# Optimization experiments

Measured on AMD Instinct MI355X. Metric: run time of the kernel, lower is better.

Reference implementation:

```python
import jax, jax.numpy as jnp
import numpy as np
from jax import lax

B, H, W, CL, CC, CD, NH, NP = 8, 48, 48, 384, 384, 384, 12, 4
N = H * W
HD = CL // NH
SCALE = HD ** -0.5


def _pool_mat(n, out=7):
    # torch AdaptiveAvgPool2d bin edges: [floor(i*n/out), ceil((i+1)*n/out))
    M = np.zeros((out, n), np.float32)
    for i in range(out):
        s = (i * n) // out
        e = -(-((i + 1) * n) // out)
        M[i, s:e] = 1.0 / (e - s)
    return jnp.asarray(M)


def _resize_mat(out_n, in_n):
    # bilinear, align_corners=False (torch F.interpolate)
    M = np.zeros((out_n, in_n), np.float32)
    scale = in_n / out_n
    for o in range(out_n):
        src = (o + 0.5) * scale - 0.5
        src = min(max(src, 0.0), in_n - 1.0)
        i0 = int(np.floor(src))
        i1 = min(i0 + 1, in_n - 1)
        f = src - i0
        M[o, i0] += 1.0 - f
        M[o, i1] += f
    return jnp.asarray(M)


def _ln_c(x, g, b):
    # LayerNorm over channel dim of NCHW, eps=1e-6
    mu = jnp.mean(x, axis=1, keepdims=True)
    var = jnp.mean((x - mu) ** 2, axis=1, keepdims=True)
    xn = (x - mu) * lax.rsqrt(var + 1e-6)
    return xn * g[None, :, None, None] + b[None, :, None, None]


def _c1(x, w):
    # 1x1 conv, w: (out,in)
    return jnp.einsum('oc,bchw->bohw', w, x)


def _bilerp(feat, grid):
    # feat (G,C,Hs,Ws), grid (G,M,2) xy in [-1,1]; align_corners=False, zero padding
    G, C, Hs, Ws = feat.shape
    x = (grid[..., 0] + 1.0) * 0.5 * Ws - 0.5
    y = (grid[..., 1] + 1.0) * 0.5 * Hs - 0.5
    x0 = jnp.floor(x)
    y0 = jnp.floor(y)
    fx = x - x0
    fy = y - y0
    featf = feat.transpose(0, 2, 3, 1).reshape(G, Hs * Ws, C)
    x0i = x0.astype(jnp.int32)
    y0i = y0.astype(jnp.int32)

    def corner(ix, iy):
        valid = ((ix >= 0) & (ix < Ws) & (iy >= 0) & (iy < Hs)).astype(feat.dtype)
        flat = jnp.clip(iy, 0, Hs - 1) * Ws + jnp.clip(ix, 0, Ws - 1)
        g = jax.vmap(lambda f, i: f[i])(featf, flat)  # (G,M,C)
        return g * valid[..., None]

    v00 = corner(x0i, y0i)
    v01 = corner(x0i + 1, y0i)
    v10 = corner(x0i, y0i + 1)
    v11 = corner(x0i + 1, y0i + 1)
    w00 = ((1 - fx) * (1 - fy))[..., None]
    w01 = (fx * (1 - fy))[..., None]
    w10 = ((1 - fx) * fy)[..., None]
    w11 = (fx * fy)[..., None]
    return v00 * w00 + v01 * w01 + v10 * w10 + v11 * w11  # (G,M,C)


def _forward(local_feat, context_prior, deformable_x, W_q, W_k, W_v, W_pre, ln1_g, ln1_b,
             W_post, dw_w, dw_b, ln2_g, ln2_b, W_lo, b_lo, W_off, b_off,
             attention_biases, W_p, bn_g, bn_b, bn_mean, bn_var):
    q = _c1(local_feat, W_q)  # (B,CL,H,W)

    # context_offset_guide: 1x1 -> GELU -> adaptive pool 7x7 -> LN(C) -> 1x1 to 32 -> resize
    cg = jax.nn.gelu(_c1(context_prior, W_pre), approximate=False)
    Mh, Mw = _pool_mat(H), _pool_mat(W)
    pooled = jnp.einsum('oh,pw,bchw->bcop', Mh, Mw, cg)
    guide = _c1(_ln_c(pooled, ln1_g, ln1_b), W_post)  # (B,32,7,7)
    Uh, Uw = _resize_mat(H, 7), _resize_mat(W, 7)
    guide = jnp.einsum('Oh,Pw,bchw->bcOP', Uh, Uw, guide)  # (B,32,H,W)

    # local_offset_base: dwconv3x3 -> LN(C) -> GELU -> 1x1 to 32
    dw = lax.conv_general_dilated(local_feat, dw_w, (1, 1), [(1, 1), (1, 1)],
                                  dimension_numbers=('NCHW', 'OIHW', 'NCHW'),
                                  feature_group_count=CL) + dw_b[None, :, None, None]
    lo = jax.nn.gelu(_ln_c(dw, ln2_g, ln2_b), approximate=False)
    lo = _c1(lo, W_lo) + b_lo[None, :, None, None]  # (B,32,H,W)

    fused = jnp.concatenate([guide, lo], axis=1)  # (B,64,H,W)
    off = _c1(fused, W_off) + b_off[None, :, None, None]  # (B,NH*NP*2,H,W)
    off = off.transpose(0, 2, 3, 1).reshape(B, H, W, NH, NP, 2)
    offn = off / jnp.asarray([W, H], dtype=off.dtype)

    ry = (jnp.arange(H, dtype=off.dtype) + 0.5) / H
    rx = (jnp.arange(W, dtype=off.dtype) + 0.5) / W
    ref = jnp.stack([jnp.broadcast_to(rx[None, :], (H, W)),
                     jnp.broadcast_to(ry[:, None], (H, W))], axis=-1)  # (H,W,2) xy
    grid = (ref[None, :, :, None, None, :] + offn) * 2.0 - 1.0  # (B,H,W,NH,NP,2)

    gridh = grid.reshape(B, N, NH, NP, 2).transpose(0, 2, 1, 3, 4)  # (B,NH,N,NP,2)
    grid_r = gridh.reshape(B * NH, N * NP, 2)

    k = _c1(context_prior, W_k).reshape(B * NH, HD, H, W)
    v = _c1(deformable_x, W_v).reshape(B * NH, HD, H, W)
    k_s = _bilerp(k, grid_r).reshape(B, NH, N, NP, HD)
    v_s = _bilerp(v, grid_r).reshape(B, NH, N, NP, HD)

    qh = q.reshape(B, NH, HD, N).transpose(0, 1, 3, 2)  # (B,NH,N,HD)
    scores = jnp.einsum('bhnd,bhnpd->bhnp', qh, k_s) * SCALE

    # relative position bias: idx(p1,p2) = |dy|*W + |dx| (first-seen enumeration)
    px = jnp.clip(jnp.round((gridh[..., 0] + 1.0) * 0.5 * W - 0.5), 0, W - 1).astype(jnp.int32)
    py = jnp.clip(jnp.round((gridh[..., 1] + 1.0) * 0.5 * H - 0.5), 0, H - 1).astype(jnp.int32)
    n = jnp.arange(N, dtype=jnp.int32)
    qy = (n // W)[None, None, :, None]
    qx = (n % W)[None, None, :, None]
    bidx = jnp.abs(qy - py) * W + jnp.abs(qx - px)  # (B,NH,N,NP)
    bias = attention_biases[jnp.arange(NH)[None, :, None, None], bidx]

    attn = jax.nn.softmax(scores + bias, axis=-1)
    out = jnp.einsum('bhnp,bhnpd->bhnd', attn, v_s)  # (B,NH,N,HD)
    out = out.transpose(0, 1, 3, 2).reshape(B, CL, H, W)

    y = _c1(out, W_p)
    y = bn_g[None, :, None, None] * (y - bn_mean[None, :, None, None]) * \
        lax.rsqrt(bn_var[None, :, None, None] + 1e-5) + bn_b[None, :, None, None]
    return y


def setup_inputs():
    ks = jax.random.split(jax.random.key(0), 16)
    f32 = jnp.float32
    d = {
        'local_feat': jax.random.normal(ks[0], (B, CL, H, W), f32),
        'context_prior': jax.random.normal(ks[1], (B, CC, H, W), f32),
        'deformable_x': jax.random.normal(ks[2], (B, CD, H, W), f32),
        'W_q': jax.random.normal(ks[3], (CL, CL), f32) * 0.02,
        'W_k': jax.random.normal(ks[4], (CL, CC), f32) * 0.02,
        'W_v': jax.random.normal(ks[5], (CD, CD), f32) * 0.02,
        'W_pre': jax.random.normal(ks[6], (CC, CC), f32) * 0.02,
        'ln1_g': jnp.ones((CC,), f32),
        'ln1_b': jnp.zeros((CC,), f32),
        'W_post': jax.random.normal(ks[7], (32, CC), f32) * 0.02,
        'dw_w': jax.random.normal(ks[8], (CL, 1, 3, 3), f32) * 0.1,
        'dw_b': jnp.zeros((CL,), f32),
        'ln2_g': jnp.ones((CL,), f32),
        'ln2_b': jnp.zeros((CL,), f32),
        'W_lo': jax.random.normal(ks[9], (32, CL), f32) * 0.02,
        'b_lo': jnp.zeros((32,), f32),
        'W_off': jax.random.normal(ks[10], (NH * NP * 2, 64), f32) * 0.01,
        'b_off': jax.random.normal(ks[11], (NH * NP * 2,), f32) * 0.5,
        'attention_biases': jax.random.normal(ks[12], (NH, H * W), f32) * 0.02,
        'W_p': jax.random.normal(ks[13], (CL, CL), f32) * 0.02,
        'bn_g': jnp.ones((CL,), f32),
        'bn_b': jnp.zeros((CL,), f32),
        'bn_mean': jax.random.normal(ks[14], (CL,), f32) * 0.01,
        'bn_var': jax.random.uniform(ks[15], (CL,), f32, 0.5, 1.5),
    }
    return d


def reference(local_feat, context_prior, deformable_x, W_q, W_k, W_v, W_pre, ln1_g, ln1_b,
              W_post, dw_w, dw_b, ln2_g, ln2_b, W_lo, b_lo, W_off, b_off,
              attention_biases, W_p, bn_g, bn_b, bn_mean, bn_var):
    return _forward(local_feat, context_prior, deformable_x, W_q, W_k, W_v, W_pre, ln1_g,
                    ln1_b, W_post, dw_w, dw_b, ln2_g, ln2_b, W_lo, b_lo, W_off, b_off,
                    attention_biases, W_p, bn_g, bn_b, bn_mean, bn_var)
```

## Files before the change

### kernel.cpp

```cpp
#include <hip/hip_runtime.h>
#include <hip/hip_bf16.h>
#include <math.h>

#define B_ 8
#define H_ 48
#define W_ 48
#define N_ 2304
#define C_ 384
#define NH_ 12
#define NP_ 4
#define HD_ 32
#define SCALE_ 0.17677669529663687f

typedef unsigned short ushort;
typedef short bf16x8 __attribute__((ext_vector_type(8)));
typedef float f32x4 __attribute__((ext_vector_type(4)));

__device__ __forceinline__ float b2f(ushort u) {
    union { float f; unsigned i; } x; x.i = ((unsigned)u) << 16; return x.f;
}
__device__ __forceinline__ ushort f2b(float f) {
    __hip_bfloat16 h = __float2bfloat16(f);
    return *(ushort*)&h;
}
__device__ __forceinline__ float ldin(const void* p, size_t i, int isbf) {
    return isbf ? b2f(((const ushort*)p)[i]) : ((const float*)p)[i];
}
__device__ __forceinline__ float geluf(float x) {
    return 0.5f * x * (1.0f + erff(x * 0.70710678118654752440f));
}
__device__ __forceinline__ int iabs(int x) { return x < 0 ? -x : x; }
__device__ __forceinline__ int get_isbf(const void* lnq) {
    return (*(const unsigned*)lnq == 0x3F803F80u) ? 1 : 0;
}

__device__ __forceinline__ void gl_lds16(const ushort* g, ushort* l) {
    __builtin_amdgcn_global_load_lds(
        (const __attribute__((address_space(1))) unsigned int*)g,
        (__attribute__((address_space(3))) unsigned int*)l, 16, 0, 0);
}

#define PREP_MAX 24
struct PrepTab {
    const void* src[PREP_MAX];
    void*       dst[PREP_MAX];
    int         n[PREP_MAX];
    int         tobf[PREP_MAX];
};
struct TPtrs { const void* src[3]; ushort* dst[3]; };
struct SetupRaw {
    const void* WoffRaw;
    const void* WloRaw;
    const void* bloRaw;
    const void* boffRaw;
    const void* dwRaw;
    const void* lnq;
    ushort* Bext;
    float*  biasp;
    float*  dwwT;
};

__global__ __launch_bounds__(256) void setup_kernel(TPtrs tp, PrepTab tab, int ne, SetupRaw rw)
{
    const int isbf = get_isbf(rw.lnq);
    const int tid = threadIdx.x;
    const int bid = blockIdx.x;
    const int DWT0 = ne * 8;
    const int WC0  = DWT0 + 2;
    const int T30  = WC0 + 96;

    if (bid < DWT0) {
        const int e = bid >> 3, sub = bid & 7;
        const int n = tab.n[e];
        const void* src = tab.src[e];
        if (tab.tobf[e]) {
            ushort* dst = (ushort*)tab.dst[e];
            if (isbf) {
                const ushort* s = (const ushort*)src;
                for (int i = sub * 256 + tid; i < n; i += 8 * 256) dst[i] = s[i];
            } else {
                const float* s = (const float*)src;
                for (int i = sub * 256 + tid; i < n; i += 8 * 256) dst[i] = f2b(s[i]);
            }
        } else {
            float* dst = (float*)tab.dst[e];
            if (isbf) {
                const ushort* s = (const ushort*)src;
                for (int i = sub * 256 + tid; i < n; i += 8 * 256) dst[i] = b2f(s[i]);
            } else {
                const float* s = (const float*)src;
                for (int i = sub * 256 + tid; i < n; i += 8 * 256) dst[i] = s[i];
            }
        }
    } else if (bid < WC0) {
        const int c = (bid - DWT0) * 256 + tid;
        if (c < C_) {
#pragma unroll
            for (int u = 0; u < 9; u++)
                rw.dwwT[u * C_ + c] = ldin(rw.dwRaw, (size_t)c * 9 + u, isbf);
        }
    } else if (bid < T30) {
        const int co = bid - WC0;
        for (int c = tid; c < C_; c += 256) {
            float acc = 0.f;
#pragma unroll 8
            for (int j = 0; j < 32; j++)
                acc += ldin(rw.WoffRaw, (size_t)co * 64 + 32 + j, isbf)
                     * ldin(rw.WloRaw, (size_t)j * 384 + c, isbf);
            ushort hi = f2b(acc);
            float r = acc - b2f(hi);
            ushort lo = f2b(r);
            rw.Bext[co * 1152 + c] = hi;
            rw.Bext[co * 1152 + 384 + c] = lo;
            rw.Bext[co * 1152 + 768 + c] = hi;
        }
        if (tid == 0) {
            float bp = ldin(rw.boffRaw, co, isbf);
            for (int j = 0; j < 32; j++)
                bp += ldin(rw.WoffRaw, (size_t)co * 64 + 32 + j, isbf)
                    * ldin(rw.bloRaw, j, isbf);
            rw.biasp[co] = bp;
        }
    } else {
        const int t3 = bid - T30;
        const int x = t3 % 36;
        const int rem = t3 / 36;
        const int y = rem % 12;
        const int z = rem / 12;
        const int which = z >> 3;
        const int b = z & 7;
        const int n0 = x * 64, c0 = y * 32;
        const void* in = tp.src[which];
        ushort* out = tp.dst[which];
        const int t = tid;

        __shared__ unsigned tile[64][33];

        if (isbf) {
            {
                const int c = t >> 3, s = t & 7;
                uint4 v = *(const uint4*)((const ushort*)in + ((size_t)b * C_ + c0 + c) * N_ + n0 + s * 8);
                const int nb = s * 8;
                tile[nb + 0][c] = v.x & 0xffff; tile[nb + 1][c] = v.x >> 16;
                tile[nb + 2][c] = v.y & 0xffff; tile[nb + 3][c] = v.y >> 16;
                tile[nb + 4][c] = v.z & 0xffff; tile[nb + 5][c] = v.z >> 16;
                tile[nb + 6][c] = v.w & 0xffff; tile[nb + 7][c] = v.w >> 16;
            }
            __syncthreads();
            {
                const int n = t >> 2, s = t & 3;
                const int cb = s * 8;
                unsigned p0 = tile[n][cb + 0] | (tile[n][cb + 1] << 16);
                unsigned p1 = tile[n][cb + 2] | (tile[n][cb + 3] << 16);
                unsigned p2 = tile[n][cb + 4] | (tile[n][cb + 5] << 16);
                unsigned p3 = tile[n][cb + 6] | (tile[n][cb + 7] << 16);
                uint4 o; o.x = p0; o.y = p1; o.z = p2; o.w = p3;
                *(uint4*)(out + ((size_t)b * N_ + n0 + n) * C_ + c0 + cb) = o;
            }
        } else {
            float* tf = (float*)&tile[0][0];
            const int tx = t & 31, ty = t >> 5;
            for (int sub = 0; sub < 2; sub++) {
                int ns = n0 + sub * 32;
                __syncthreads();
#pragma unroll
                for (int u = 0; u < 4; u++) {
                    int c = ty + u * 8;
                    tf[c * 33 + tx] = ((const float*)in)[((size_t)b * C_ + c0 + c) * N_ + ns + tx];
                }
                __syncthreads();
#pragma unroll
                for (int u = 0; u < 4; u++) {
                    int n = ty + u * 8;
                    out[((size_t)b * N_ + ns + n) * C_ + c0 + tx] = f2b(tf[tx * 33 + n]);
                }
            }
        }
    }
}

struct QKV4Ptrs { const ushort* A[4]; const ushort* Bw[4]; void* Y[4]; };
__global__ __launch_bounds__(256, 3) void mega_gemm_kernel(
    QKV4Ptrs qp,
    const ushort* __restrict__ AHI, const ushort* __restrict__ ALO,
    const ushort* __restrict__ Bext, float* __restrict__ OFFP)
{
    __shared__ ushort As[3][128 * 32];
    __shared__ ushort Bs[3][128 * 32];
    const int tid = threadIdx.x;
    const int lane = tid & 63, wave = tid >> 6;
    const int wr = wave >> 1, wc = wave & 1;
    const int quad = lane >> 4, l15 = lane & 15;
    const int bid = blockIdx.x;

    if (bid < 144) {
        const int m0 = bid * 128;

        f32x4 acc[4][3];
#pragma unroll
        for (int i = 0; i < 4; i++)
#pragma unroll
            for (int j = 0; j < 3; j++) acc[i][j] = (f32x4){0.f, 0.f, 0.f, 0.f};

        auto stage = [&](int p, int t) {
            const int seg = t / 12;
            const ushort* Ag = (seg < 2) ? AHI : ALO;
            const int acol = t * 32 - seg * 384;
            const int bcol = t * 32;
#pragma unroll
            for (int u = 0; u < 2; u++) {
                int idx = tid + 256 * u;
                int r = idx >> 2, s = idx & 3;
                int rb = r < 96 ? r : 95;
                gl_lds16(Ag + (size_t)(m0 + r) * 384 + acol + 8 * s, &As[p][idx * 8]);
                gl_lds16(Bext + (size_t)rb * 1152 + bcol + 8 * s, &Bs[p][idx * 8]);
            }
        };

        stage(0, 0);
        stage(1, 1);
        const int nt = 36;
        for (int t = 0; t < nt; ++t) {
            if (t + 1 < nt) asm volatile("s_waitcnt vmcnt(4)" ::: "memory");
            else            asm volatile("s_waitcnt vmcnt(0)" ::: "memory");
            __builtin_amdgcn_s_barrier();
            __builtin_amdgcn_sched_barrier(0);
            if (t + 2 < nt) stage((t + 2) % 3, t + 2);
            const int p = t % 3;
            bf16x8 af[4], bfr[3];
#pragma unroll
            for (int i = 0; i < 4; i++)
                af[i]  = *(const bf16x8*)&As[p][(wr * 64 + i * 16 + l15) * 32 + quad * 8];
#pragma unroll
            for (int j = 0; j < 3; j++)
                bfr[j] = *(const bf16x8*)&Bs[p][(wc * 48 + j * 16 + l15) * 32 + quad * 8];
#pragma unroll
            for (int i = 0; i < 4; i++)
#pragma unroll
                for (int j = 0; j < 3; j++)
                    acc[i][j] = __builtin_amdgcn_mfma_f32_16x16x32_bf16(af[i], bfr[j], acc[i][j], 0, 0, 0);
        }

#pragma unroll
        for (int i = 0; i < 4; i++) {
#pragma unroll
            for (int r = 0; r < 4; r++) {
                int m = m0 + wr * 64 + i * 16 + quad * 4 + r;
#pragma unroll
                for (int j = 0; j < 3; j++) {
                    int co = wc * 48 + j * 16 + l15;
                    OFFP[(size_t)m * 96 + co] = acc[i][j][r];
                }
            }
        }
    } else {
        const int q = bid - 144;
        const int zc = q / 54, r2 = q % 54;
        const int which = zc >> 3, b = zc & 7;
        const int m0 = (r2 / 3) * 128;
        const int n0 = (r2 % 3) * 128;
        const ushort* Ag = qp.A[which];
        const ushort* Bg = qp.Bw[which];

        f32x4 acc[4][4];
#pragma unroll
        for (int i = 0; i < 4; i++)
#pragma unroll
            for (int j = 0; j < 4; j++) acc[i][j] = (f32x4){0.f, 0.f, 0.f, 0.f};

        const size_t abase = (size_t)b * (size_t)N_ * C_;

        auto stage = [&](int p, int kc) {
#pragma unroll
            for (int u = 0; u < 2; u++) {
                int idx = tid + 256 * u;
                int r = idx >> 2, s = idx & 3;
                gl_lds16(Ag + abase + (size_t)(m0 + r) * C_ + kc + 8 * s, &As[p][idx * 8]);
                gl_lds16(Bg + (size_t)(n0 + r) * C_ + kc + 8 * s, &Bs[p][idx * 8]);
            }
        };

        stage(0, 0);
        stage(1, 32);
        const int nt = C_ / 32;
        for (int t = 0; t < nt; ++t) {
            if (t + 1 < nt) asm volatile("s_waitcnt vmcnt(4)" ::: "memory");
            else            asm volatile("s_waitcnt vmcnt(0)" ::: "memory");
            __builtin_amdgcn_s_barrier();
            __builtin_amdgcn_sched_barrier(0);
            if (t + 2 < nt) stage((t + 2) % 3, (t + 2) * 32);
            const int p = t % 3;
            bf16x8 af[4], bfr[4];
#pragma unroll
            for (int i = 0; i < 4; i++)
                af[i]  = *(const bf16x8*)&As[p][(wr * 64 + i * 16 + l15) * 32 + quad * 8];
#pragma unroll
            for (int j = 0; j < 4; j++)
                bfr[j] = *(const bf16x8*)&Bs[p][(wc * 64 + j * 16 + l15) * 32 + quad * 8];
#pragma unroll
            for (int i = 0; i < 4; i++)
#pragma unroll
                for (int j = 0; j < 4; j++)
                    acc[i][j] = __builtin_amdgcn_mfma_f32_16x16x32_bf16(af[i], bfr[j], acc[i][j], 0, 0, 0);
        }

        ushort* Yg = (ushort*)qp.Y[which];
        if (which < 3) {
#pragma unroll
            for (int i = 0; i < 4; i++) {
#pragma unroll
                for (int r = 0; r < 4; r++) {
                    int m = m0 + wr * 64 + i * 16 + quad * 4 + r;
#pragma unroll
                    for (int j = 0; j < 4; j++) {
                        int nn = n0 + wc * 64 + j * 16 + l15;
                        Yg[abase + (size_t)m * C_ + nn] = f2b(acc[i][j][r]);
                    }
                }
            }
        } else {
#pragma unroll
            for (int i = 0; i < 4; i++) {
#pragma unroll
                for (int r = 0; r < 4; r++) {
                    int m = m0 + wr * 64 + i * 16 + quad * 4 + r;
#pragma unroll
                    for (int j = 0; j < 4; j++) {
                        int nn = n0 + wc * 64 + j * 16 + l15;
                        Yg[abase + (size_t)m * C_ + nn] = f2b(geluf(acc[i][j][r]));
                    }
                }
            }
        }
    }
}

__global__ __launch_bounds__(256, 4) void gemm_final_kernel(
    const ushort* __restrict__ WpB, const ushort* __restrict__ AOut,
    void* __restrict__ Yg,
    const float* __restrict__ bng, const float* __restrict__ bnb,
    const float* __restrict__ bnm, const float* __restrict__ bnv,
    const void* __restrict__ lnq)
{
    const int isbf = get_isbf(lnq);
    const int l = (blockIdx.x & 7) * 108 + (blockIdx.x >> 3);
    const int b = l / 108, r2 = l % 108;
    const int n0 = (r2 / 3) * 64;
    const int m0 = (r2 % 3) * 128;

    __shared__ ushort As[3][128 * 32];
    __shared__ ushort Bs[3][64 * 32];
    const int tid = threadIdx.x;
    const int lane = tid & 63, wave = tid >> 6;
    const int quad = lane >> 4, l15 = lane & 15;
    const int sx = (quad ^ (l15 & 3)) * 8;

    f32x4 acc[2][4];
#pragma unroll
    for (int i = 0; i < 2; i++)
#pragma unroll
        for (int j = 0; j < 4; j++) acc[i][j] = (f32x4){0.f, 0.f, 0.f, 0.f};

    const size_t bbase = (size_t)b * (size_t)N_ * C_;

    auto stage = [&](int p, int kc) {
#pragma unroll
        for (int u = 0; u < 2; u++) {
            int idx = tid + 256 * u;
            int r = idx >> 2, sl = idx & 3;
            int sg = sl ^ (r & 3);
            gl_lds16(WpB + (size_t)(m0 + r) * C_ + kc + 8 * sg, &As[p][idx * 8]);
        }
        {
            int r = tid >> 2, sl = tid & 3;
            int sg = sl ^ (r & 3);
            gl_lds16(AOut + bbase + (size_t)(n0 + r) * C_ + kc + 8 * sg, &Bs[p][tid * 8]);
        }
    };

    stage(0, 0);
    stage(1, 32);

    const int nt = C_ / 32;
    for (int t = 0; t < nt; ++t) {
        if (t + 1 < nt) asm volatile("s_waitcnt vmcnt(3)" ::: "memory");
        else            asm volatile("s_waitcnt vmcnt(0)" ::: "memory");
        __builtin_amdgcn_s_barrier();
        __builtin_amdgcn_sched_barrier(0);
        if (t + 2 < nt) stage((t + 2) % 3, (t + 2) * 32);
        const int p = t % 3;
        bf16x8 af[2], bfr[4];
#pragma unroll
        for (int i = 0; i < 2; i++)
            af[i]  = *(const bf16x8*)&As[p][(wave * 32 + i * 16 + l15) * 32 + sx];
#pragma unroll
        for (int j = 0; j < 4; j++)
            bfr[j] = *(const bf16x8*)&Bs[p][(j * 16 + l15) * 32 + sx];
#pragma unroll
        for (int i = 0; i < 2; i++)
#pragma unroll
            for (int j = 0; j < 4; j++)
                acc[i][j] = __builtin_amdgcn_mfma_f32_16x16x32_bf16(af[i], bfr[j], acc[i][j], 0, 0, 0);
    }

    const size_t ybase = (size_t)b * (size_t)C_ * N_;
#pragma unroll
    for (int i = 0; i < 2; i++) {
#pragma unroll
        for (int r = 0; r < 4; r++) {
            int m = m0 + wave * 32 + i * 16 + quad * 4 + r;
            float sc = bng[m] * rsqrtf(bnv[m] + 1e-5f);
            float sh = bnb[m] - sc * bnm[m];
#pragma unroll
            for (int j = 0; j < 4; j++) {
                int nn = n0 + j * 16 + l15;
                float v = sc * acc[i][j][r] + sh;
                size_t yi = ybase + (size_t)m * N_ + nn;
                if (isbf) ((ushort*)Yg)[yi] = f2b(v);
                else ((float*)Yg)[yi] = v;
            }
        }
    }
}

__global__ __launch_bounds__(384) void pool_ln_guide_kernel(
    const ushort* __restrict__ CG, const float* __restrict__ g, const float* __restrict__ bt,
    const ushort* __restrict__ WpostB, const ushort* __restrict__ WoffB,
    float* __restrict__ OG7)
{
    const int cell = blockIdx.x % 49, b = blockIdx.x / 49;
    const int i = cell / 7, j = cell % 7, c = threadIdx.x;
    const int sh = (i * H_) / 7, eh = ((i + 1) * H_ + 6) / 7;
    const int sw = (j * W_) / 7, ew = ((j + 1) * W_ + 6) / 7;
    float s = 0.f;
    for (int h = sh; h < eh; h++)
        for (int w = sw; w < ew; w++)
            s += b2f(CG[((size_t)b * N_ + h * W_ + w) * C_ + c]);
    s *= 1.0f / (float)((eh - sh) * (ew - sw));

    float rs = s, rq = s * s;
#pragma unroll
    for (int m = 1; m <= 32; m <<= 1) {
        rs += __shfl_xor(rs, m);
        rq += __shfl_xor(rq, m);
    }
    __shared__ float ss[6], sq[6], buf[C_];
    __shared__ float psum[12][33];
    __shared__ float g7s[32];
    int wid = threadIdx.x >> 6;
    if ((threadIdx.x & 63) == 0) { ss[wid] = rs; sq[wid] = rq; }
    __syncthreads();
    if (threadIdx.x == 0) {
        float ts = 0.f, tq = 0.f;
        for (int k = 0; k < 6; k++) { ts += ss[k]; tq += sq[k]; }
        ss[0] = ts; sq[0] = tq;
    }
    __syncthreads();
    float mu = ss[0] / (float)C_;
    float var = sq[0] / (float)C_ - mu * mu;
    float inv = rsqrtf(var + 1e-6f);
    buf[c] = (s - mu) * inv * g[c] + bt[c];
    __syncthreads();

    const int oc = threadIdx.x & 31, seg = threadIdx.x >> 5;
    const uint4* wp = (const uint4*)(WpostB + oc * C_ + seg * 32);
    float part = 0.f;
#pragma unroll
    for (int u = 0; u < 4; u++) {
        uint4 v = wp[u];
        const float* bb = &buf[seg * 32 + u * 8];
        part += b2f((ushort)(v.x & 0xffff)) * bb[0] + b2f((ushort)(v.x >> 16)) * bb[1];
        part += b2f((ushort)(v.y & 0xffff)) * bb[2] + b2f((ushort)(v.y >> 16)) * bb[3];
        part += b2f((ushort)(v.z & 0xffff)) * bb[4] + b2f((ushort)(v.z >> 16)) * bb[5];
        part += b2f((ushort)(v.w & 0xffff)) * bb[6] + b2f((ushort)(v.w >> 16)) * bb[7];
    }
    psum[seg][oc] = part;
    __syncthreads();
    if (threadIdx.x < 32) {
        float acc = 0.f;
#pragma unroll
        for (int k = 0; k < 12; k++) acc += psum[k][threadIdx.x];
        g7s[threadIdx.x] = acc;
    }
    __syncthreads();
    if (threadIdx.x < 96) {
        const int co = threadIdx.x;
        float acc = 0.f;
#pragma unroll 8
        for (int k = 0; k < 32; k++)
            acc += b2f(WoffB[co * 64 + k]) * g7s[k];
        OG7[(size_t)blockIdx.x * 96 + co] = acc;
    }
}

__global__ __launch_bounds__(512) void dw_ln_gelu_kernel(
    const ushort* __restrict__ LF, const float* __restrict__ WdT, const float* __restrict__ BdF,
    const float* __restrict__ g, const float* __restrict__ bt,
    ushort* __restrict__ AHI, ushort* __restrict__ ALO)
{
    const int wave = threadIdx.x >> 6, lane = threadIdx.x & 63;
    const int m = blockIdx.x * 8 + wave;
    const int b = m / N_, n = m % N_;
    const int h = n / W_, w = n % W_;
    const bool act = lane < 48;
    const int c0 = lane * 8;

    float acc[8];
#pragma unroll
    for (int j = 0; j < 8; j++) acc[j] = 0.f;
    if (act) {
        f32x4 b0 = *(const f32x4*)(BdF + c0);
        f32x4 b1 = *(const f32x4*)(BdF + c0 + 4);
#pragma unroll
        for (int j = 0; j < 4; j++) { acc[j] = b0[j]; acc[4 + j] = b1[j]; }
    }

#pragma unroll
    for (int u = 0; u < 9; u++) {
        const int ky = u / 3, kx = u % 3;
        const int y = h + ky - 1, x = w + kx - 1;
        if (act && y >= 0 && y < H_ && x >= 0 && x < W_) {
            uint4 v = *(const uint4*)(LF + ((size_t)b * N_ + y * W_ + x) * C_ + c0);
            f32x4 wa = *(const f32x4*)(WdT + u * C_ + c0);
            f32x4 wb = *(const f32x4*)(WdT + u * C_ + c0 + 4);
            acc[0] += wa[0] * b2f((ushort)(v.x & 0xffff));
            acc[1] += wa[1] * b2f((ushort)(v.x >> 16));
            acc[2] += wa[2] * b2f((ushort)(v.y & 0xffff));
            acc[3] += wa[3] * b2f((ushort)(v.y >> 16));
            acc[4] += wb[0] * b2f((ushort)(v.z & 0xffff));
            acc[5] += wb[1] * b2f((ushort)(v.z >> 16));
            acc[6] += wb[2] * b2f((ushort)(v.w & 0xffff));
            acc[7] += wb[3] * b2f((ushort)(v.w >> 16));
        }
    }

    float rs = 0.f, rq = 0.f;
#pragma unroll
    for (int j = 0; j < 8; j++) { rs += acc[j]; rq += acc[j] * acc[j]; }
#pragma unroll
    for (int s = 1; s <= 32; s <<= 1) {
        rs += __shfl_xor(rs, s);
        rq += __shfl_xor(rq, s);
    }
    float mu = rs / (float)C_;
    float var = rq / (float)C_ - mu * mu;
    float inv = rsqrtf(var + 1e-6f);

    if (act) {
        f32x4 g0 = *(const f32x4*)(g + c0);
        f32x4 g1 = *(const f32x4*)(g + c0 + 4);
        f32x4 t0 = *(const f32x4*)(bt + c0);
        f32x4 t1 = *(const f32x4*)(bt + c0 + 4);
        float v[8];
#pragma unroll
        for (int j = 0; j < 4; j++) {
            v[j]     = geluf((acc[j]     - mu) * inv * g0[j] + t0[j]);
            v[4 + j] = geluf((acc[4 + j] - mu) * inv * g1[j] + t1[j]);
        }
        uint4 hi, lo;
        ushort hs[8], ls[8];
#pragma unroll
        for (int j = 0; j < 8; j++) {
            hs[j] = f2b(v[j]);
            ls[j] = f2b(v[j] - b2f(hs[j]));
        }
        hi.x = (unsigned)hs[0] | ((unsigned)hs[1] << 16);
        hi.y = (unsigned)hs[2] | ((unsigned)hs[3] << 16);
        hi.z = (unsigned)hs[4] | ((unsigned)hs[5] << 16);
        hi.w = (unsigned)hs[6] | ((unsigned)hs[7] << 16);
        lo.x = (unsigned)ls[0] | ((unsigned)ls[1] << 16);
        lo.y = (unsigned)ls[2] | ((unsigned)ls[3] << 16);
        lo.z = (unsigned)ls[4] | ((unsigned)ls[5] << 16);
        lo.w = (unsigned)ls[6] | ((unsigned)ls[7] << 16);
        size_t idx = (size_t)m * C_ + c0;
        *(uint4*)(AHI + idx) = hi;
        *(uint4*)(ALO + idx) = lo;
    }
}

__global__ __launch_bounds__(384) void attn_kernel(
    const ushort* __restrict__ Q, const ushort* __restrict__ K, const ushort* __restrict__ V,
    const float* __restrict__ OFFP, const float* __restrict__ biasp,
    const float* __restrict__ OG7,
    const float* __restrict__ ABf, ushort* __restrict__ OUT)
{
    const int pairi = blockIdx.x;
    const int b = pairi / (N_ / 2);
    const int n0 = (pairi % (N_ / 2)) * 2;
    const int tid = threadIdx.x;

    __shared__ int   cidxS[96][4];
    __shared__ float cwS[96][4];
    __shared__ float biasS[96];

    if (tid < 96) {
        const int pos = tid / 48, idx = tid % 48;
        const int n = n0 + pos;
        const int h = n / W_, w = n % W_;
        const int nh = idx >> 2, p = idx & 3;
        const int co = nh * 8 + 2 * p;

        const float fs = 7.0f / 48.0f;
        float sy = fminf(fmaxf(((float)h + 0.5f) * fs - 0.5f, 0.f), 6.f);
        float sx = fminf(fmaxf(((float)w + 0.5f) * fs - 0.5f, 0.f), 6.f);
        int gy0 = (int)floorf(sy), gx0 = (int)floorf(sx);
        int gy1 = min(gy0 + 1, 6), gx1 = min(gx0 + 1, 6);
        float gfy = sy - (float)gy0, gfx = sx - (float)gx0;
        float bw00 = (1.f - gfy) * (1.f - gfx), bw01 = (1.f - gfy) * gfx;
        float bw10 = gfy * (1.f - gfx), bw11 = gfy * gfx;
        const float* ogb = OG7 + (size_t)b * 49 * 96;
        int c00 = (gy0 * 7 + gx0) * 96, c01 = (gy0 * 7 + gx1) * 96;
        int c10 = (gy1 * 7 + gx0) * 96, c11 = (gy1 * 7 + gx1) * 96;
        const size_t mrow = ((size_t)b * N_ + n) * 96;

        float ox = OFFP[mrow + co] + biasp[co]
                 + bw00 * ogb[c00 + co] + bw01 * ogb[c01 + co]
                 + bw10 * ogb[c10 + co] + bw11 * ogb[c11 + co];
        float oy = OFFP[mrow + co + 1] + biasp[co + 1]
                 + bw00 * ogb[c00 + co + 1] + bw01 * ogb[c01 + co + 1]
                 + bw10 * ogb[c10 + co + 1] + bw11 * ogb[c11 + co + 1];

        float x = (float)w + ox;
        float y = (float)h + oy;

        int px = (int)fminf(fmaxf(rintf(x), 0.f), (float)(W_ - 1));
        int py = (int)fminf(fmaxf(rintf(y), 0.f), (float)(H_ - 1));
        biasS[tid] = ABf[(size_t)nh * N_ + iabs(h - py) * W_ + iabs(w - px)];

        float x0f = floorf(x), y0f = floorf(y);
        float fx = x - x0f, fy = y - y0f;
        int x0 = (int)x0f, y0 = (int)y0f;
#pragma unroll
        for (int cc = 0; cc < 4; cc++) {
            int dx = cc & 1, dy = cc >> 1;
            int ix = x0 + dx, iy = y0 + dy;
            bool valid = (ix >= 0) && (ix < W_) && (iy >= 0) && (iy < H_);
            int ixc = min(max(ix, 0), W_ - 1), iyc = min(max(iy, 0), H_ - 1);
            cidxS[tid][cc] = iyc * W_ + ixc;
            float wx = dx ? fx : (1.f - fx);
            float wy = dy ? fy : (1.f - fy);
            cwS[tid][cc] = valid ? wx * wy : 0.f;
        }
    }
    __syncthreads();

    const int pos = tid / 192, r = tid % 192;
    const int nh = r >> 4, dd = r & 15;
    const int n = n0 + pos;
    const size_t row = ((size_t)b * N_ + n) * C_ + nh * HD_ + dd * 2;
    unsigned qu = *(const unsigned*)(Q + row);
    const float q0 = b2f((ushort)(qu & 0xffff));
    const float q1 = b2f((ushort)(qu >> 16));
    const size_t kvbase = (size_t)b * N_ * C_ + nh * HD_ + dd * 2;
    const int s0 = pos * 48 + nh * 4;

    int   ci[NP_][4];
    float cw[NP_][4];
#pragma unroll
    for (int p = 0; p < NP_; p++)
#pragma unroll
        for (int cc = 0; cc < 4; cc++) {
            ci[p][cc] = cidxS[s0 + p][cc];
            cw[p][cc] = cwS[s0 + p][cc];
        }

    float sc[NP_];
#pragma unroll
    for (int p = 0; p < NP_; p++) {
        float ks0 = 0.f, ks1 = 0.f;
#pragma unroll
        for (int cc = 0; cc < 4; cc++) {
            unsigned kv = *(const unsigned*)(K + kvbase + (size_t)ci[p][cc] * C_);
            ks0 += cw[p][cc] * b2f((ushort)(kv & 0xffff));
            ks1 += cw[p][cc] * b2f((ushort)(kv >> 16));
        }
        float dot = q0 * ks0 + q1 * ks1;
#pragma unroll
        for (int m = 1; m <= 8; m <<= 1) dot += __shfl_xor(dot, m);
        sc[p] = dot * SCALE_ + biasS[s0 + p];
    }

    float m = fmaxf(fmaxf(sc[0], sc[1]), fmaxf(sc[2], sc[3]));
    float e[NP_], esum = 0.f;
#pragma unroll
    for (int p = 0; p < NP_; p++) { e[p] = __expf(sc[p] - m); esum += e[p]; }
    float inv = 1.0f / esum;

    float o0 = 0.f, o1 = 0.f;
#pragma unroll
    for (int p = 0; p < NP_; p++) {
        float vs0 = 0.f, vs1 = 0.f;
#pragma unroll
        for (int cc = 0; cc < 4; cc++) {
            unsigned vv = *(const unsigned*)(V + kvbase + (size_t)ci[p][cc] * C_);
            vs0 += cw[p][cc] * b2f((ushort)(vv & 0xffff));
            vs1 += cw[p][cc] * b2f((ushort)(vv >> 16));
        }
        float ep = e[p] * inv;
        o0 += ep * vs0;
        o1 += ep * vs1;
    }
    unsigned ou = (unsigned)f2b(o0) | ((unsigned)f2b(o1) << 16);
    *(unsigned*)(OUT + row) = ou;
}

extern "C" void kernel_launch(void* const* d_in, const int* in_sizes, int n_in,
                              void* d_out, int out_size, void* d_ws, size_t ws_size,
                              hipStream_t stream)
{
    const void* local_feat    = d_in[0];
    const void* context_prior = d_in[1];
    const void* deformable_x  = d_in[2];

    const size_t BIGE = (size_t)B_ * N_ * C_;

    char* wsb = (char*)d_ws;
    auto carve = [&](size_t bytes) { char* p = wsb; wsb += (bytes + 255) & ~(size_t)255; return p; };
    int*    flag = (int*)carve(256);
    ushort* T1   = (ushort*)carve(BIGE * 2);
    ushort* T2   = (ushort*)carve(BIGE * 2);
    ushort* T3   = (ushort*)carve(BIGE * 2);
    ushort* Qb   = (ushort*)carve(BIGE * 2);
    ushort* Kb   = (ushort*)carve(BIGE * 2);
    ushort* Vb   = (ushort*)carve(BIGE * 2);
    ushort* AHI  = (ushort*)carve(BIGE * 2);
    ushort* ALO  = (ushort*)carve(BIGE * 2);
    ushort* CGB  = (ushort*)carve(BIGE * 2);
    ushort* AOut = (ushort*)carve(BIGE * 2);
    float*  OFFB = (float*)carve((size_t)B_ * N_ * 96 * 4);
    ushort* WqB   = (ushort*)carve(147456 * 2);
    ushort* WkB   = (ushort*)carve(147456 * 2);
    ushort* WvB   = (ushort*)carve(147456 * 2);
    ushort* WpreB = (ushort*)carve(147456 * 2);
    ushort* WpB   = (ushort*)carve(147456 * 2);
    ushort* WpostB= (ushort*)carve(12288 * 2);
    ushort* WoffB = (ushort*)carve(6144 * 2);
    ushort* Bext  = (ushort*)carve(96 * 1152 * 2);
    float*  biasp = (float*)carve(96 * 4);
    float*  OG7   = (float*)carve((size_t)B_ * 49 * 96 * 4);
    float*  dwwT  = (float*)carve(3456 * 4);
    float*  ABf   = (float*)carve(27648 * 4);
    float*  dwbF  = (float*)carve(384 * 4);
    float*  ln1gF = (float*)carve(384 * 4);
    float*  ln1bF = (float*)carve(384 * 4);
    float*  ln2gF = (float*)carve(384 * 4);
    float*  ln2bF = (float*)carve(384 * 4);
    float*  bngF  = (float*)carve(384 * 4);
    float*  bnbF  = (float*)carve(384 * 4);
    float*  bnmF  = (float*)carve(384 * 4);
    float*  bnvF  = (float*)carve(384 * 4);
    (void)flag;

    PrepTab tab;
    int ne = 0;
    auto add = [&](const void* s, void* d, int n, int tb) {
        tab.src[ne] = s; tab.dst[ne] = d; tab.n[ne] = n; tab.tobf[ne] = tb; ne++;
    };
    add(d_in[3],  WqB,   147456, 1);
    add(d_in[4],  WkB,   147456, 1);
    add(d_in[5],  WvB,   147456, 1);
    add(d_in[6],  WpreB, 147456, 1);
    add(d_in[19], WpB,   147456, 1);
    add(d_in[9],  WpostB, 12288, 1);
    add(d_in[16], WoffB,   6144, 1);
    add(d_in[18], ABf,    27648, 0);
    add(d_in[11], dwbF,     384, 0);
    add(d_in[7],  ln1gF,    384, 0);
    add(d_in[8],  ln1bF,    384, 0);
    add(d_in[12], ln2gF,    384, 0);
    add(d_in[13], ln2bF,    384, 0);
    add(d_in[20], bngF,     384, 0);
    add(d_in[21], bnbF,     384, 0);
    add(d_in[22], bnmF,     384, 0);
    add(d_in[23], bnvF,     384, 0);

    TPtrs tp;
    tp.src[0] = local_feat;    tp.dst[0] = T1;
    tp.src[1] = context_prior; tp.dst[1] = T2;
    tp.src[2] = deformable_x;  tp.dst[2] = T3;

    SetupRaw rw;
    rw.WoffRaw = d_in[16];
    rw.WloRaw  = d_in[14];
    rw.bloRaw  = d_in[15];
    rw.boffRaw = d_in[17];
    rw.dwRaw   = d_in[10];
    rw.lnq     = d_in[7];
    rw.Bext    = Bext;
    rw.biasp   = biasp;
    rw.dwwT    = dwwT;

    const int setup_blocks = ne * 8 + 2 + 96 + 10368;
    setup_kernel<<<setup_blocks, 256, 0, stream>>>(tp, tab, ne, rw);

    dim3 blk256(256);

    dw_ln_gelu_kernel<<<(B_ * N_) / 8, 512, 0, stream>>>(T1, dwwT, dwbF, ln2gF, ln2bF, AHI, ALO);

    QKV4Ptrs qp;
    qp.A[0] = T1; qp.Bw[0] = WqB;   qp.Y[0] = Qb;
    qp.A[1] = T2; qp.Bw[1] = WkB;   qp.Y[1] = Kb;
    qp.A[2] = T3; qp.Bw[2] = WvB;   qp.Y[2] = Vb;
    qp.A[3] = T2; qp.Bw[3] = WpreB; qp.Y[3] = CGB;
    mega_gemm_kernel<<<1872, blk256, 0, stream>>>(qp, AHI, ALO, Bext, OFFB);

    pool_ln_guide_kernel<<<B_ * 49, 384, 0, stream>>>(CGB, ln1gF, ln1bF, WpostB, WoffB, OG7);

    attn_kernel<<<(B_ * N_) / 2, 384, 0, stream>>>(Qb, Kb, Vb, OFFB, biasp, OG7, ABf, AOut);

    gemm_final_kernel<<<864, blk256, 0, stream>>>(
        WpB, AOut, d_out, bngF, bnbF, bnmF, bnvF, d_in[7]);
}
```

Baseline: 331.7 us.

## Fuse K and pre-projection GEMMs sharing input T2 into one block

The K projection and the W_pre projection both read activation T2, so each tile is now computed by a single block that loads the A tile once and runs two accumulator sets against two weight tiles, writing K and GELU(CG). This removes 432 blocks and halves the A-tile global traffic for those two GEMMs. The fused path uses double buffering with a third LDS slot for the second weight, adds an extra barrier per k-step, and doubles accumulator registers, so launch bounds drop to 2 blocks per SM, which lowers occupancy for every path of the kernel.

```diff
diff --git a/kernel.cpp b/kernel.cpp
--- a/kernel.cpp
+++ b/kernel.cpp
@@ -180,7 +180,7 @@
 }
 
 struct QKV4Ptrs { const ushort* A[4]; const ushort* Bw[4]; void* Y[4]; };
-__global__ __launch_bounds__(256, 3) void mega_gemm_kernel(
+__global__ __launch_bounds__(256, 2) void mega_gemm_kernel(
     QKV4Ptrs qp,
     const ushort* __restrict__ AHI, const ushort* __restrict__ ALO,
     const ushort* __restrict__ Bext, float* __restrict__ OFFP)
@@ -253,22 +253,27 @@
                 }
             }
         }
-    } else {
-        const int q = bid - 144;
-        const int zc = q / 54, r2 = q % 54;
-        const int which = zc >> 3, b = zc & 7;
-        const int m0 = (r2 / 3) * 128;
-        const int n0 = (r2 % 3) * 128;
-        const ushort* Ag = qp.A[which];
-        const ushort* Bg = qp.Bw[which];
+        return;
+    }
+
+    const int u0 = bid - 144;
+    const int kind = u0 / 432;
+    const int rr = u0 % 432;
+    const int b = rr / 54, r2 = rr % 54;
+    const int m0 = (r2 / 3) * 128;
+    const int n0 = (r2 % 3) * 128;
+    const size_t abase = (size_t)b * (size_t)N_ * C_;
+
+    if (kind != 1) {
+        const ushort* Ag = qp.A[kind];
+        const ushort* Bg = qp.Bw[kind];
+        ushort* Yg = (ushort*)qp.Y[kind];
 
         f32x4 acc[4][4];
 #pragma unroll
         for (int i = 0; i < 4; i++)
 #pragma unroll
             for (int j = 0; j < 4; j++) acc[i][j] = (f32x4){0.f, 0.f, 0.f, 0.f};
-
-        const size_t abase = (size_t)b * (size_t)N_ * C_;
 
         auto stage = [&](int p, int kc) {
 #pragma unroll
@@ -304,31 +309,91 @@
                     acc[i][j] = __builtin_amdgcn_mfma_f32_16x16x32_bf16(af[i], bfr[j], acc[i][j], 0, 0, 0);
         }
 
-        ushort* Yg = (ushort*)qp.Y[which];
-        if (which < 3) {
-#pragma unroll
-            for (int i = 0; i < 4; i++) {
-#pragma unroll
-                for (int r = 0; r < 4; r++) {
-                    int m = m0 + wr * 64 + i * 16 + quad * 4 + r;
-#pragma unroll
-                    for (int j = 0; j < 4; j++) {
-                        int nn = n0 + wc * 64 + j * 16 + l15;
-                        Yg[abase + (size_t)m * C_ + nn] = f2b(acc[i][j][r]);
-                    }
+#pragma unroll
+        for (int i = 0; i < 4; i++) {
+#pragma unroll
+            for (int r = 0; r < 4; r++) {
+                int m = m0 + wr * 64 + i * 16 + quad * 4 + r;
+#pragma unroll
+                for (int j = 0; j < 4; j++) {
+                    int nn = n0 + wc * 64 + j * 16 + l15;
+                    Yg[abase + (size_t)m * C_ + nn] = f2b(acc[i][j][r]);
                 }
             }
-        } else {
-#pragma unroll
-            for (int i = 0; i < 4; i++) {
-#pragma unroll
-                for (int r = 0; r < 4; r++) {
-                    int m = m0 + wr * 64 + i * 16 + quad * 4 + r;
-#pragma unroll
-                    for (int j = 0; j < 4; j++) {
-                        int nn = n0 + wc * 64 + j * 16 + l15;
-                        Yg[abase + (size_t)m * C_ + nn] = f2b(geluf(acc[i][j][r]));
-                    }
+        }
+    } else {
+        const ushort* Ag = qp.A[1];
+        const ushort* Bk = qp.Bw[1];
+        const ushort* Bc = qp.Bw[3];
+        ushort* Yk = (ushort*)qp.Y[1];
+        ushort* Yc = (ushort*)qp.Y[3];
+
+        ushort* Cs0 = &As[2][0];
+        ushort* Cs1 = &Bs[2][0];
+
+        f32x4 acck[4][4], accc[4][4];
+#pragma unroll
+        for (int i = 0; i < 4; i++)
+#pragma unroll
+            for (int j = 0; j < 4; j++) {
+                acck[i][j] = (f32x4){0.f, 0.f, 0.f, 0.f};
+                accc[i][j] = (f32x4){0.f, 0.f, 0.f, 0.f};
+            }
+
+        auto stage = [&](int p, int kc) {
+            ushort* Cs = p ? Cs1 : Cs0;
+#pragma unroll
+            for (int u = 0; u < 2; u++) {
+                int idx = tid + 256 * u;
+                int r = idx >> 2, s = idx & 3;
+                gl_lds16(Ag + abase + (size_t)(m0 + r) * C_ + kc + 8 * s, &As[p][idx * 8]);
+                gl_lds16(Bk + (size_t)(n0 + r) * C_ + kc + 8 * s, &Bs[p][idx * 8]);
+                gl_lds16(Bc + (size_t)(n0 + r) * C_ + kc + 8 * s, &Cs[idx * 8]);
+            }
+        };
+
+        stage(0, 0);
+        const int nt = C_ / 32;
+        for (int t = 0; t < nt; ++t) {
+            if (t + 1 < nt) {
+                stage((t + 1) & 1, (t + 1) * 32);
+                asm volatile("s_waitcnt vmcnt(6)" ::: "memory");
+            } else {
+                asm volatile("s_waitcnt vmcnt(0)" ::: "memory");
+            }
+            __builtin_amdgcn_s_barrier();
+            __builtin_amdgcn_sched_barrier(0);
+            const int p = t & 1;
+            const ushort* Cs = p ? Cs1 : Cs0;
+            bf16x8 af[4], bfr[4], cfr[4];
+#pragma unroll
+            for (int i = 0; i < 4; i++)
+                af[i]  = *(const bf16x8*)&As[p][(wr * 64 + i * 16 + l15) * 32 + quad * 8];
+#pragma unroll
+            for (int j = 0; j < 4; j++) {
+                bfr[j] = *(const bf16x8*)&Bs[p][(wc * 64 + j * 16 + l15) * 32 + quad * 8];
+                cfr[j] = *(const bf16x8*)&Cs[(wc * 64 + j * 16 + l15) * 32 + quad * 8];
+            }
+#pragma unroll
+            for (int i = 0; i < 4; i++)
+#pragma unroll
+                for (int j = 0; j < 4; j++) {
+                    acck[i][j] = __builtin_amdgcn_mfma_f32_16x16x32_bf16(af[i], bfr[j], acck[i][j], 0, 0, 0);
+                    accc[i][j] = __builtin_amdgcn_mfma_f32_16x16x32_bf16(af[i], cfr[j], accc[i][j], 0, 0, 0);
+                }
+            __builtin_amdgcn_s_barrier();
+        }
+
+#pragma unroll
+        for (int i = 0; i < 4; i++) {
+#pragma unroll
+            for (int r = 0; r < 4; r++) {
+                int m = m0 + wr * 64 + i * 16 + quad * 4 + r;
+#pragma unroll
+                for (int j = 0; j < 4; j++) {
+                    int nn = n0 + wc * 64 + j * 16 + l15;
+                    Yk[abase + (size_t)m * C_ + nn] = f2b(acck[i][j][r]);
+                    Yc[abase + (size_t)m * C_ + nn] = f2b(geluf(accc[i][j][r]));
                 }
             }
         }
@@ -802,7 +867,7 @@
     qp.A[1] = T2; qp.Bw[1] = WkB;   qp.Y[1] = Kb;
     qp.A[2] = T3; qp.Bw[2] = WvB;   qp.Y[2] = Vb;
     qp.A[3] = T2; qp.Bw[3] = WpreB; qp.Y[3] = CGB;
-    mega_gemm_kernel<<<1872, blk256, 0, stream>>>(qp, AHI, ALO, Bext, OFFB);
+    mega_gemm_kernel<<<1440, blk256, 0, stream>>>(qp, AHI, ALO, Bext, OFFB);
 
     pool_ln_guide_kernel<<<B_ * 49, 384, 0, stream>>>(CGB, ln1gF, ln1bF, WpostB, WoffB, OG7);
 
```

Measured after the change: 328.4 us. Within noise of the previous version (-1.0%).
